# Optimization experiments

Hardware: AMD Instinct MI355X
Metric: run time of the kernel (lower is better)

The kernel has to match this reference:

```python
import jax, jax.numpy as jnp
import numpy as np

B, S, D, H = 4, 2048, 1024, 16
HD = D // H


def setup_inputs() -> dict:
    key = jax.random.key(0)
    ks = jax.random.split(key, 6)
    s = 1.0 / np.sqrt(D)
    return {
        "x": jax.random.normal(ks[0], (B, S, D), dtype=jnp.float32),
        "Wq": jax.random.normal(ks[1], (D, D), dtype=jnp.float32) * s,
        "Wk": jax.random.normal(ks[2], (D, D), dtype=jnp.float32) * s,
        "Wv": jax.random.normal(ks[3], (D, D), dtype=jnp.float32) * s,
        "Wo": jax.random.normal(ks[4], (D, D), dtype=jnp.float32) * s,
        "bo": jnp.zeros((D,), dtype=jnp.float32),
    }


def reference(x, Wq, Wk, Wv, Wo, bo):
    b, n, d = x.shape
    # QKV projections (torch Linear: x @ W.T, but weights here are stored as [d_in, d_out])
    q = (x @ Wq).reshape(b, n, H, HD).transpose(0, 2, 1, 3)  # [b,h,n,hd]
    k = (x @ Wk).reshape(b, n, H, HD).transpose(0, 2, 1, 3)
    v = (x @ Wv).reshape(b, n, H, HD).transpose(0, 2, 1, 3)
    scores = jnp.einsum("bhqd,bhkd->bhqk", q, k) / np.sqrt(HD)
    causal = jnp.tril(jnp.ones((n, n), dtype=bool))  # True = keep
    scores = jnp.where(causal, scores, -jnp.inf)
    attn = jax.nn.softmax(scores, axis=-1)
    ctx = jnp.einsum("bhqk,bhkd->bhqd", attn, v)
    ctx = ctx.transpose(0, 2, 1, 3).reshape(b, n, d)
    return ctx @ Wo + bo
```

## Files before the change

kernel.cpp:

```cpp
#include <hip/hip_runtime.h>
#include <hip/hip_bf16.h>

typedef __bf16 bf16;
typedef __bf16 bf16x4 __attribute__((ext_vector_type(4)));
typedef __bf16 bf16x8 __attribute__((ext_vector_type(8)));
typedef float f32x4 __attribute__((ext_vector_type(4)));

static constexpr int Bn = 4, Sn = 2048, Dn = 1024, Hn = 16, HDn = 64;
static constexpr int Mn = Bn * Sn;

__device__ __forceinline__ void gload_lds16(const void* g, void* l) {
  __builtin_amdgcn_global_load_lds(
      (const __attribute__((address_space(1))) unsigned int*)g,
      (__attribute__((address_space(3))) unsigned int*)l, 16, 0, 0);
}

__global__ void cvt_x_kernel(const float* __restrict__ x, bf16* __restrict__ xb, int n8) {
  int i = blockIdx.x * blockDim.x + threadIdx.x;
  if (i >= n8) return;
  const float4* p = reinterpret_cast<const float4*>(x) + (size_t)i * 2;
  float4 a = p[0], b = p[1];
  bf16x8 v;
  v[0] = (bf16)a.x; v[1] = (bf16)a.y; v[2] = (bf16)a.z; v[3] = (bf16)a.w;
  v[4] = (bf16)b.x; v[5] = (bf16)b.y; v[6] = (bf16)b.z; v[7] = (bf16)b.w;
  *(reinterpret_cast<bf16x8*>(xb) + i) = v;
}

struct alignas(8) B4 { bf16 e[4]; };

__global__ void transpose_w_kernel(const float* __restrict__ W0, const float* __restrict__ W1,
                                   const float* __restrict__ W2, const float* __restrict__ W3,
                                   bf16* __restrict__ WtQKV, bf16* __restrict__ Wot) {
  __shared__ bf16 tile[64][65];
  const int which = blockIdx.z;
  const float* W = (which == 0) ? W0 : (which == 1) ? W1 : (which == 2) ? W2 : W3;
  bf16* out = (which < 3) ? (WtQKV + (size_t)which * 1024 * 1024) : Wot;
  const int k0 = blockIdx.y * 64, n0 = blockIdx.x * 64;
  const int t = threadIdx.x;
  const int tr = t >> 4, tc = (t & 15) * 4;
#pragma unroll
  for (int rr = 0; rr < 4; ++rr) {
    const int row = rr * 16 + tr;
    float4 v = *reinterpret_cast<const float4*>(&W[(size_t)(k0 + row) * 1024 + n0 + tc]);
    tile[row][tc + 0] = (bf16)v.x; tile[row][tc + 1] = (bf16)v.y;
    tile[row][tc + 2] = (bf16)v.z; tile[row][tc + 3] = (bf16)v.w;
  }
  __syncthreads();
#pragma unroll
  for (int rr = 0; rr < 4; ++rr) {
    const int row = rr * 16 + tr;
    B4 o;
#pragma unroll
    for (int j = 0; j < 4; ++j) o.e[j] = tile[tc + j][row];
    *reinterpret_cast<B4*>(&out[(size_t)(n0 + row) * 1024 + k0 + tc]) = o;
  }
}

template <int MODE>
__global__ __launch_bounds__(256, 4)
void gemm_kernel(const bf16* __restrict__ A, const bf16* __restrict__ Bt,
                 float* __restrict__ Co, const float* __restrict__ bias,
                 bf16* __restrict__ Qo, bf16* __restrict__ Ko, bf16* __restrict__ Vto) {
  __shared__ bf16 Al[128 * 64];
  __shared__ bf16 Bl[128 * 64];
  const int tid = threadIdx.x;
  const int lane = tid & 63;
  const int wv = tid >> 6;
  const int wm = wv >> 1, wn = wv & 1;
  const int lr = lane & 15, lg = lane >> 4;
  const int m0 = blockIdx.y * 128, n0 = blockIdx.x * 128;

  int soff[4];
  const bf16* srcA[4];
  const bf16* srcB[4];
#pragma unroll
  for (int it = 0; it < 4; ++it) {
    const int elem = it * 2048 + tid * 8;
    const int row = elem >> 6;
    const int g = (elem >> 3) & 7;
    const int gs = g ^ (row & 7);
    soff[it] = elem;
    srcA[it] = A + (size_t)(m0 + row) * 1024 + gs * 8;
    srcB[it] = Bt + (size_t)(n0 + row) * 1024 + gs * 8;
  }

  f32x4 acc[4][4] = {};

  for (int ks = 0; ks < 16; ++ks) {
    const int kn = ks * 64;
#pragma unroll
    for (int it = 0; it < 4; ++it) {
      gload_lds16(srcA[it] + kn, (bf16*)&Al[0] + soff[it]);
      gload_lds16(srcB[it] + kn, (bf16*)&Bl[0] + soff[it]);
    }
    __syncthreads();
#pragma unroll
    for (int kk = 0; kk < 2; ++kk) {
      bf16x8 af[4], bfr[4];
#pragma unroll
      for (int i = 0; i < 4; ++i) {
        const int row = wm * 64 + i * 16 + lr;
        af[i] = *reinterpret_cast<const bf16x8*>(Al + row * 64 + (((kk * 4 + lg) ^ (row & 7)) << 3));
      }
#pragma unroll
      for (int i = 0; i < 4; ++i) {
        const int row = wn * 64 + i * 16 + lr;
        bfr[i] = *reinterpret_cast<const bf16x8*>(Bl + row * 64 + (((kk * 4 + lg) ^ (row & 7)) << 3));
      }
#pragma unroll
      for (int mi = 0; mi < 4; ++mi)
#pragma unroll
        for (int ni = 0; ni < 4; ++ni)
          acc[mi][ni] = __builtin_amdgcn_mfma_f32_16x16x32_bf16(af[mi], bfr[ni], acc[mi][ni], 0, 0, 0);
    }
    __syncthreads();
  }

  const int mrow = lg * 4;
  if (MODE == 0) {
    const int w = n0 >> 10;
    const int nl0 = n0 & 1023;
    if (w == 2) {
      const int b = m0 >> 11;
      const int sBase = (m0 & 2047) + wm * 64 + lg * 8;
#pragma unroll
      for (int ni = 0; ni < 4; ++ni) {
        const int nl = nl0 + wn * 64 + ni * 16 + lr;
        const int h = nl >> 6, hd = nl & 63;
        bf16* vbase = Vto + ((size_t)(b * 16 + h) * 64 + hd) * 2048;
#pragma unroll
        for (int mi = 0; mi < 4; ++mi) {
          B4 o;
#pragma unroll
          for (int i = 0; i < 4; ++i) o.e[i] = (bf16)acc[mi][ni][i];
          const int sNew = sBase + ((mi >> 1) << 5) + ((mi & 1) << 2);
          *reinterpret_cast<B4*>(&vbase[sNew]) = o;
        }
      }
    } else {
      const float fs = (w == 0) ? 0.18033688011112042f : 1.0f;
#pragma unroll
      for (int ni = 0; ni < 4; ++ni) {
        const int nl = nl0 + wn * 64 + ni * 16 + lr;
        const int h = nl >> 6, hd = nl & 63;
        bf16* dst = (w == 0) ? Qo : Ko;
#pragma unroll
        for (int mi = 0; mi < 4; ++mi) {
#pragma unroll
          for (int i = 0; i < 4; ++i) {
            const int m_g = m0 + wm * 64 + mi * 16 + mrow + i;
            const int b = m_g >> 11, s = m_g & 2047;
            dst[((size_t)(b * 16 + h) * 2048 + s) * 64 + hd] = (bf16)(acc[mi][ni][i] * fs);
          }
        }
      }
    }
  } else {
#pragma unroll
    for (int ni = 0; ni < 4; ++ni) {
      const int n_g = n0 + wn * 64 + ni * 16 + lr;
      const float bv = bias[n_g];
#pragma unroll
      for (int mi = 0; mi < 4; ++mi) {
#pragma unroll
        for (int i = 0; i < 4; ++i) {
          const int m_g = m0 + wm * 64 + mi * 16 + mrow + i;
          Co[(size_t)m_g * 1024 + n_g] = acc[mi][ni][i] + bv;
        }
      }
    }
  }
}

__device__ __forceinline__ unsigned int pack2(float lo, float hi) {
  union { bf16 bb[2]; unsigned int u; } c;
  c.bb[0] = (bf16)lo; c.bb[1] = (bf16)hi;
  return c.u;
}

__device__ __forceinline__ float smax_pack(const f32x4 (&sc)[4], unsigned int (&pk)[4][2],
                                           int kv0, int qrow, bool domask, int lg) {
  float p[4][4];
  float rs = 0.f;
#pragma unroll
  for (int ni = 0; ni < 4; ++ni)
#pragma unroll
    for (int r = 0; r < 4; ++r) {
      float pv = __builtin_amdgcn_exp2f(sc[ni][r]);
      if (domask && (kv0 + ni * 16 + lg * 4 + r > qrow)) pv = 0.f;
      p[ni][r] = pv;
      rs += pv;
    }
#pragma unroll
  for (int ni = 0; ni < 4; ++ni)
#pragma unroll
    for (int tt = 0; tt < 2; ++tt)
      pk[ni][tt] = pack2(p[ni][2 * tt], p[ni][2 * tt + 1]);
  return rs;
}

__global__ __launch_bounds__(256, 4)
void attn_kernel(const bf16* __restrict__ Q, const bf16* __restrict__ K,
                 const bf16* __restrict__ Vt, bf16* __restrict__ ctx) {
  __shared__ bf16 Kl[2][4096];
  __shared__ bf16 Vl[2][4096];
  const int tid = threadIdx.x, lane = tid & 63, wv = tid >> 6;
  const int lr = lane & 15, lg = lane >> 4, lk = lg * 8;
  const int bid = blockIdx.x;
  const int xcd = bid & 7, slot = bid >> 3;
  const int bh = xcd * 8 + (slot >> 4);
  const int pi = slot & 15;
  const bf16* Qh = Q + (size_t)bh * Sn * 64;
  const bf16* Kh = K + (size_t)bh * Sn * 64;
  const bf16* Vh = Vt + (size_t)bh * 64 * (size_t)Sn;
  const int b = bh >> 4, h = bh & 15;

  const int e0 = tid * 8, e1 = 2048 + tid * 8;
  const int r0 = e0 >> 6, r1 = e1 >> 6;
  const int gs0 = ((e0 >> 3) & 7) ^ (r0 & 7), gs1 = ((e1 >> 3) & 7) ^ (r1 & 7);
  const bf16* srcK0 = Kh + r0 * 64 + gs0 * 8;
  const bf16* srcK1 = Kh + r1 * 64 + gs1 * 8;
  const bf16* srcV0 = Vh + (size_t)r0 * Sn + gs0 * 8;
  const bf16* srcV1 = Vh + (size_t)r1 * Sn + gs1 * 8;

  for (int ph = 0; ph < 2; ++ph) {
    const int qtile = ph ? pi : 31 - pi;
    const int qw = qtile * 64 + wv * 16;
    const int qrow = qw + lr;
    bf16x8 aq[2];
#pragma unroll
    for (int kk = 0; kk < 2; ++kk)
      aq[kk] = *reinterpret_cast<const bf16x8*>(&Qh[(size_t)(qw + lr) * 64 + kk * 32 + lk]);

    f32x4 acc[4] = {};
    float lst = 0.f;
    const int nt = qtile + 1;

    gload_lds16(srcK0, &Kl[0][e0]);
    gload_lds16(srcK1, &Kl[0][e1]);
    gload_lds16(srcV0, &Vl[0][e0]);
    gload_lds16(srcV1, &Vl[0][e1]);
    __syncthreads();

    for (int t = 0; t < nt; ++t) {
      const int cur = t & 1;
      if (t + 1 < nt) {
        const int kvn = (t + 1) * 64;
        gload_lds16(srcK0 + kvn * 64, &Kl[cur ^ 1][e0]);
        gload_lds16(srcK1 + kvn * 64, &Kl[cur ^ 1][e1]);
        gload_lds16(srcV0 + kvn, &Vl[cur ^ 1][e0]);
        gload_lds16(srcV1 + kvn, &Vl[cur ^ 1][e1]);
      }
      const int kv0 = t * 64;
      const bf16* KlF = Kl[cur];
      const bf16* VlF = Vl[cur];

      f32x4 sc[4] = {};
#pragma unroll
      for (int kk = 0; kk < 2; ++kk) {
        bf16x8 ak[4];
#pragma unroll
        for (int ni = 0; ni < 4; ++ni) {
          const int row = ni * 16 + lr;
          ak[ni] = *reinterpret_cast<const bf16x8*>(KlF + row * 64 + (((kk * 4 + lg) ^ (row & 7)) << 3));
        }
        __builtin_amdgcn_s_setprio(1);
#pragma unroll
        for (int ni = 0; ni < 4; ++ni)
          sc[ni] = __builtin_amdgcn_mfma_f32_16x16x32_bf16(ak[ni], aq[kk], sc[ni], 0, 0, 0);
        __builtin_amdgcn_s_setprio(0);
      }
      unsigned int pk[4][2];
      {
        float rs = smax_pack(sc, pk, kv0, qrow, t == nt - 1, lg);
        rs += __shfl_xor(rs, 16);
        rs += __shfl_xor(rs, 32);
        lst += rs;
      }
#pragma unroll
      for (int kk = 0; kk < 2; ++kk) {
        union { unsigned int u[4]; bf16x8 v; } ap;
#pragma unroll
        for (int w = 0; w < 4; ++w) ap.u[w] = pk[2 * kk + (w >> 1)][w & 1];
        __builtin_amdgcn_s_setprio(1);
#pragma unroll
        for (int ni = 0; ni < 4; ++ni) {
          const int row = ni * 16 + lr;
          bf16x8 av = *reinterpret_cast<const bf16x8*>(VlF + row * 64 + (((kk * 4 + lg) ^ (row & 7)) << 3));
          acc[ni] = __builtin_amdgcn_mfma_f32_16x16x32_bf16(av, ap.v, acc[ni], 0, 0, 0);
        }
        __builtin_amdgcn_s_setprio(0);
      }
      __syncthreads();
    }

    const float inv = 1.f / lst;
    bf16* cbase = ctx + (((size_t)b * Sn + qw + lr) * 16 + h) * 64;
#pragma unroll
    for (int ni = 0; ni < 4; ++ni) {
      B4 o;
#pragma unroll
      for (int r = 0; r < 4; ++r) o.e[r] = (bf16)(acc[ni][r] * inv);
      *reinterpret_cast<B4*>(cbase + ni * 16 + lg * 4) = o;
    }
    __syncthreads();
  }
}

extern "C" void kernel_launch(void* const* d_in, const int* in_sizes, int n_in,
                              void* d_out, int out_size, void* d_ws, size_t ws_size,
                              hipStream_t stream) {
  const float* x = (const float*)d_in[0];
  const float* Wq = (const float*)d_in[1];
  const float* Wk = (const float*)d_in[2];
  const float* Wv = (const float*)d_in[3];
  const float* Wo = (const float*)d_in[4];
  const float* bo = (const float*)d_in[5];

  char* ws = (char*)d_ws;
  bf16* xb    = (bf16*)(ws);
  bf16* WtQKV = (bf16*)(ws + 0x1000000);
  bf16* Wot   = (bf16*)(ws + 0x1600000);
  bf16* Qb    = (bf16*)(ws + 0x1800000);
  bf16* Kb    = (bf16*)(ws + 0x2800000);
  bf16* Vtb   = (bf16*)(ws + 0x3800000);
  bf16* ctx   = xb;

  cvt_x_kernel<<<dim3(Mn * Dn / 8 / 256), dim3(256), 0, stream>>>(x, xb, Mn * Dn / 8);
  transpose_w_kernel<<<dim3(16, 16, 4), dim3(256), 0, stream>>>(Wq, Wk, Wv, Wo, WtQKV, Wot);
  gemm_kernel<0><<<dim3(24, 64), dim3(256), 0, stream>>>(xb, WtQKV, nullptr, nullptr, Qb, Kb, Vtb);
  attn_kernel<<<dim3(1024), dim3(256), 0, stream>>>(Qb, Kb, Vtb, ctx);
  gemm_kernel<1><<<dim3(8, 64), dim3(256), 0, stream>>>(ctx, Wot, (float*)d_out, bo,
                                                        nullptr, nullptr, nullptr);
}
```

Before: 160.4 us.

## Split KV tiles across waves with LDS reduction of partial attention outputs

Each of the four waves now handles all 64 query rows of the tile but only every fourth KV tile, instead of each wave owning 16 query rows and sweeping all KV tiles. Four KV tiles are staged into LDS per group, and at the end the partial accumulators and row sums are merged through a padded shared buffer. This lets each wave reuse its K/V fragments across four query sub-blocks and cuts the number of barriers per KV tile. In exchange it needs much more LDS (about 69KB) and more registers, so occupancy is lowered to 2 blocks per CU, there is no prefetch overlap between groups, and a reduction step is added. The softmax is unnormalized without a running max, so partial sums can be added directly.

```diff
diff --git a/kernel.cpp b/kernel.cpp
--- a/kernel.cpp
+++ b/kernel.cpp
@@ -199,11 +199,14 @@
   return rs;
 }
 
-__global__ __launch_bounds__(256, 4)
+__global__ __launch_bounds__(256, 2)
 void attn_kernel(const bf16* __restrict__ Q, const bf16* __restrict__ K,
                  const bf16* __restrict__ Vt, bf16* __restrict__ ctx) {
-  __shared__ bf16 Kl[2][4096];
-  __shared__ bf16 Vl[2][4096];
+  __shared__ char smem[70656];
+  bf16* stg = (bf16*)smem;
+  float* mrgF = (float*)smem;
+  float* lstb = (float*)(smem + 69632);
+
   const int tid = threadIdx.x, lane = tid & 63, wv = tid >> 6;
   const int lr = lane & 15, lg = lane >> 4, lk = lg * 8;
   const int bid = blockIdx.x;
@@ -225,83 +228,110 @@
 
   for (int ph = 0; ph < 2; ++ph) {
     const int qtile = ph ? pi : 31 - pi;
-    const int qw = qtile * 64 + wv * 16;
-    const int qrow = qw + lr;
-    bf16x8 aq[2];
-#pragma unroll
-    for (int kk = 0; kk < 2; ++kk)
-      aq[kk] = *reinterpret_cast<const bf16x8*>(&Qh[(size_t)(qw + lr) * 64 + kk * 32 + lk]);
-
-    f32x4 acc[4] = {};
-    float lst = 0.f;
+    const int q0 = qtile * 64;
+    bf16x8 aq[4][2];
+#pragma unroll
+    for (int qs = 0; qs < 4; ++qs)
+#pragma unroll
+      for (int kk = 0; kk < 2; ++kk)
+        aq[qs][kk] = *reinterpret_cast<const bf16x8*>(
+            &Qh[(size_t)(q0 + qs * 16 + lr) * 64 + kk * 32 + lk]);
+
+    f32x4 acc[4][4] = {};
+    float lst[4] = {0.f, 0.f, 0.f, 0.f};
     const int nt = qtile + 1;
-
-    gload_lds16(srcK0, &Kl[0][e0]);
-    gload_lds16(srcK1, &Kl[0][e1]);
-    gload_lds16(srcV0, &Vl[0][e0]);
-    gload_lds16(srcV1, &Vl[0][e1]);
+    const int ng = (nt + 3) >> 2;
+
+    for (int g = 0; g < ng; ++g) {
+#pragma unroll
+      for (int sl = 0; sl < 4; ++sl) {
+        int tw = 4 * g + sl;
+        tw = (tw < nt) ? tw : 0;
+        bf16* db = stg + sl * 8192;
+        gload_lds16(srcK0 + (size_t)tw * 4096, db + e0);
+        gload_lds16(srcK1 + (size_t)tw * 4096, db + e1);
+        gload_lds16(srcV0 + tw * 64, db + 4096 + e0);
+        gload_lds16(srcV1 + tw * 64, db + 4096 + e1);
+      }
+      __syncthreads();
+
+      const int t = 4 * g + wv;
+      if (t < nt) {
+        const bf16* KlF = stg + wv * 8192;
+        const bf16* VlF = KlF + 4096;
+        bf16x8 ak[2][4], av[2][4];
+#pragma unroll
+        for (int kk = 0; kk < 2; ++kk)
+#pragma unroll
+          for (int ni = 0; ni < 4; ++ni) {
+            const int row = ni * 16 + lr;
+            const int off = row * 64 + (((kk * 4 + lg) ^ (row & 7)) << 3);
+            ak[kk][ni] = *reinterpret_cast<const bf16x8*>(KlF + off);
+            av[kk][ni] = *reinterpret_cast<const bf16x8*>(VlF + off);
+          }
+        const int kv0 = t * 64;
+        const bool domask = (t == nt - 1);
+#pragma unroll
+        for (int qs = 0; qs < 4; ++qs) {
+          const int qrow = q0 + qs * 16 + lr;
+          f32x4 sc[4] = {};
+          __builtin_amdgcn_s_setprio(1);
+#pragma unroll
+          for (int kk = 0; kk < 2; ++kk)
+#pragma unroll
+            for (int ni = 0; ni < 4; ++ni)
+              sc[ni] = __builtin_amdgcn_mfma_f32_16x16x32_bf16(ak[kk][ni], aq[qs][kk], sc[ni], 0, 0, 0);
+          __builtin_amdgcn_s_setprio(0);
+          unsigned int pk[4][2];
+          float rs = smax_pack(sc, pk, kv0, qrow, domask, lg);
+          rs += __shfl_xor(rs, 16);
+          rs += __shfl_xor(rs, 32);
+          lst[qs] += rs;
+          __builtin_amdgcn_s_setprio(1);
+#pragma unroll
+          for (int kk = 0; kk < 2; ++kk) {
+            union { unsigned int u[4]; bf16x8 v; } ap;
+#pragma unroll
+            for (int w = 0; w < 4; ++w) ap.u[w] = pk[2 * kk + (w >> 1)][w & 1];
+#pragma unroll
+            for (int ni = 0; ni < 4; ++ni)
+              acc[qs][ni] = __builtin_amdgcn_mfma_f32_16x16x32_bf16(av[kk][ni], ap.v, acc[qs][ni], 0, 0, 0);
+          }
+          __builtin_amdgcn_s_setprio(0);
+        }
+      }
+      __syncthreads();
+    }
+
+#pragma unroll
+    for (int qs = 0; qs < 4; ++qs) {
+      float* rowp = mrgF + (size_t)(wv * 64 + qs * 16 + lr) * 68;
+#pragma unroll
+      for (int ni = 0; ni < 4; ++ni)
+        *reinterpret_cast<f32x4*>(rowp + ni * 16 + lg * 4) = acc[qs][ni];
+    }
+    if (lg == 0) {
+#pragma unroll
+      for (int qs = 0; qs < 4; ++qs) lstb[wv * 64 + qs * 16 + lr] = lst[qs];
+    }
     __syncthreads();
-
-    for (int t = 0; t < nt; ++t) {
-      const int cur = t & 1;
-      if (t + 1 < nt) {
-        const int kvn = (t + 1) * 64;
-        gload_lds16(srcK0 + kvn * 64, &Kl[cur ^ 1][e0]);
-        gload_lds16(srcK1 + kvn * 64, &Kl[cur ^ 1][e1]);
-        gload_lds16(srcV0 + kvn, &Vl[cur ^ 1][e0]);
-        gload_lds16(srcV1 + kvn, &Vl[cur ^ 1][e1]);
-      }
-      const int kv0 = t * 64;
-      const bf16* KlF = Kl[cur];
-      const bf16* VlF = Vl[cur];
-
-      f32x4 sc[4] = {};
-#pragma unroll
-      for (int kk = 0; kk < 2; ++kk) {
-        bf16x8 ak[4];
-#pragma unroll
-        for (int ni = 0; ni < 4; ++ni) {
-          const int row = ni * 16 + lr;
-          ak[ni] = *reinterpret_cast<const bf16x8*>(KlF + row * 64 + (((kk * 4 + lg) ^ (row & 7)) << 3));
-        }
-        __builtin_amdgcn_s_setprio(1);
-#pragma unroll
-        for (int ni = 0; ni < 4; ++ni)
-          sc[ni] = __builtin_amdgcn_mfma_f32_16x16x32_bf16(ak[ni], aq[kk], sc[ni], 0, 0, 0);
-        __builtin_amdgcn_s_setprio(0);
-      }
-      unsigned int pk[4][2];
-      {
-        float rs = smax_pack(sc, pk, kv0, qrow, t == nt - 1, lg);
-        rs += __shfl_xor(rs, 16);
-        rs += __shfl_xor(rs, 32);
-        lst += rs;
-      }
-#pragma unroll
-      for (int kk = 0; kk < 2; ++kk) {
-        union { unsigned int u[4]; bf16x8 v; } ap;
-#pragma unroll
-        for (int w = 0; w < 4; ++w) ap.u[w] = pk[2 * kk + (w >> 1)][w & 1];
-        __builtin_amdgcn_s_setprio(1);
-#pragma unroll
-        for (int ni = 0; ni < 4; ++ni) {
-          const int row = ni * 16 + lr;
-          bf16x8 av = *reinterpret_cast<const bf16x8*>(VlF + row * 64 + (((kk * 4 + lg) ^ (row & 7)) << 3));
-          acc[ni] = __builtin_amdgcn_mfma_f32_16x16x32_bf16(av, ap.v, acc[ni], 0, 0, 0);
-        }
-        __builtin_amdgcn_s_setprio(0);
-      }
-      __syncthreads();
-    }
-
-    const float inv = 1.f / lst;
-    bf16* cbase = ctx + (((size_t)b * Sn + qw + lr) * 16 + h) * 64;
-#pragma unroll
-    for (int ni = 0; ni < 4; ++ni) {
-      B4 o;
-#pragma unroll
-      for (int r = 0; r < 4; ++r) o.e[r] = (bf16)(acc[ni][r] * inv);
-      *reinterpret_cast<B4*>(cbase + ni * 16 + lg * 4) = o;
+    {
+      const int qloc = wv * 16 + lr;
+      const float lt = lstb[qloc] + lstb[64 + qloc] + lstb[128 + qloc] + lstb[192 + qloc];
+      const float inv = 1.f / lt;
+      bf16* cbase = ctx + (((size_t)b * Sn + q0 + qloc) * 16 + h) * 64;
+#pragma unroll
+      for (int ni = 0; ni < 4; ++ni) {
+        const int hoff = ni * 16 + lg * 4;
+        f32x4 s = *reinterpret_cast<const f32x4*>(mrgF + (size_t)qloc * 68 + hoff);
+#pragma unroll
+        for (int pw = 1; pw < 4; ++pw)
+          s += *reinterpret_cast<const f32x4*>(mrgF + (size_t)(pw * 64 + qloc) * 68 + hoff);
+        B4 o;
+#pragma unroll
+        for (int r = 0; r < 4; ++r) o.e[r] = (bf16)(s[r] * inv);
+        *reinterpret_cast<B4*>(cbase + hoff) = o;
+      }
     }
     __syncthreads();
   }
```

New measurement: 178.5 us. +11.3%, slower.

## Give each attention wave two query sub-tiles to reuse K/V fragments

Applied to the files above, without the earlier changes.

The attention kernel drops from four waves to two per block. Each wave now handles two 16-row query sub-tiles, so every K and V fragment read from LDS feeds two MFMAs. Each thread issues four async loads per buffer instead of two to fill the same K/V tile. This halves LDS read traffic per MFMA, at the cost of more registers per wave, fewer waves to hide latency, and a lower occupancy hint in launch_bounds.

```diff
diff --git a/kernel.cpp b/kernel.cpp
--- a/kernel.cpp
+++ b/kernel.cpp
@@ -199,7 +199,7 @@
   return rs;
 }
 
-__global__ __launch_bounds__(256, 4)
+__global__ __launch_bounds__(128, 2)
 void attn_kernel(const bf16* __restrict__ Q, const bf16* __restrict__ K,
                  const bf16* __restrict__ Vt, bf16* __restrict__ ctx) {
   __shared__ bf16 Kl[2][4096];
@@ -215,93 +215,120 @@
   const bf16* Vh = Vt + (size_t)bh * 64 * (size_t)Sn;
   const int b = bh >> 4, h = bh & 15;
 
-  const int e0 = tid * 8, e1 = 2048 + tid * 8;
-  const int r0 = e0 >> 6, r1 = e1 >> 6;
-  const int gs0 = ((e0 >> 3) & 7) ^ (r0 & 7), gs1 = ((e1 >> 3) & 7) ^ (r1 & 7);
-  const bf16* srcK0 = Kh + r0 * 64 + gs0 * 8;
-  const bf16* srcK1 = Kh + r1 * 64 + gs1 * 8;
-  const bf16* srcV0 = Vh + (size_t)r0 * Sn + gs0 * 8;
-  const bf16* srcV1 = Vh + (size_t)r1 * Sn + gs1 * 8;
+  int eo[4];
+  const bf16* sK[4];
+  const bf16* sV[4];
+#pragma unroll
+  for (int c = 0; c < 4; ++c) {
+    const int e = c * 1024 + tid * 8;
+    const int row = e >> 6;
+    const int gs = ((e >> 3) & 7) ^ (row & 7);
+    eo[c] = e;
+    sK[c] = Kh + row * 64 + gs * 8;
+    sV[c] = Vh + (size_t)row * Sn + gs * 8;
+  }
 
   for (int ph = 0; ph < 2; ++ph) {
     const int qtile = ph ? pi : 31 - pi;
-    const int qw = qtile * 64 + wv * 16;
-    const int qrow = qw + lr;
-    bf16x8 aq[2];
-#pragma unroll
-    for (int kk = 0; kk < 2; ++kk)
-      aq[kk] = *reinterpret_cast<const bf16x8*>(&Qh[(size_t)(qw + lr) * 64 + kk * 32 + lk]);
-
-    f32x4 acc[4] = {};
-    float lst = 0.f;
+    const int q0 = qtile * 64;
+    const int qw = q0 + wv * 16;
+    bf16x8 aq[2][2];
+#pragma unroll
+    for (int sub = 0; sub < 2; ++sub)
+#pragma unroll
+      for (int kk = 0; kk < 2; ++kk)
+        aq[sub][kk] = *reinterpret_cast<const bf16x8*>(
+            &Qh[(size_t)(qw + sub * 32 + lr) * 64 + kk * 32 + lk]);
+
+    f32x4 acc[2][4] = {};
+    float lst[2] = {0.f, 0.f};
     const int nt = qtile + 1;
 
-    gload_lds16(srcK0, &Kl[0][e0]);
-    gload_lds16(srcK1, &Kl[0][e1]);
-    gload_lds16(srcV0, &Vl[0][e0]);
-    gload_lds16(srcV1, &Vl[0][e1]);
+#pragma unroll
+    for (int c = 0; c < 4; ++c) {
+      gload_lds16(sK[c], &Kl[0][eo[c]]);
+      gload_lds16(sV[c], &Vl[0][eo[c]]);
+    }
     __syncthreads();
 
     for (int t = 0; t < nt; ++t) {
       const int cur = t & 1;
       if (t + 1 < nt) {
         const int kvn = (t + 1) * 64;
-        gload_lds16(srcK0 + kvn * 64, &Kl[cur ^ 1][e0]);
-        gload_lds16(srcK1 + kvn * 64, &Kl[cur ^ 1][e1]);
-        gload_lds16(srcV0 + kvn, &Vl[cur ^ 1][e0]);
-        gload_lds16(srcV1 + kvn, &Vl[cur ^ 1][e1]);
+#pragma unroll
+        for (int c = 0; c < 4; ++c) {
+          gload_lds16(sK[c] + (size_t)kvn * 64, &Kl[cur ^ 1][eo[c]]);
+          gload_lds16(sV[c] + kvn, &Vl[cur ^ 1][eo[c]]);
+        }
       }
       const int kv0 = t * 64;
       const bf16* KlF = Kl[cur];
       const bf16* VlF = Vl[cur];
-
-      f32x4 sc[4] = {};
-#pragma unroll
-      for (int kk = 0; kk < 2; ++kk) {
-        bf16x8 ak[4];
+      const bool domask = (t == nt - 1);
+
+      bf16x8 ak[2][4];
+#pragma unroll
+      for (int kk = 0; kk < 2; ++kk)
 #pragma unroll
         for (int ni = 0; ni < 4; ++ni) {
           const int row = ni * 16 + lr;
-          ak[ni] = *reinterpret_cast<const bf16x8*>(KlF + row * 64 + (((kk * 4 + lg) ^ (row & 7)) << 3));
-        }
-        __builtin_amdgcn_s_setprio(1);
-#pragma unroll
-        for (int ni = 0; ni < 4; ++ni)
-          sc[ni] = __builtin_amdgcn_mfma_f32_16x16x32_bf16(ak[ni], aq[kk], sc[ni], 0, 0, 0);
-        __builtin_amdgcn_s_setprio(0);
-      }
-      unsigned int pk[4][2];
+          ak[kk][ni] = *reinterpret_cast<const bf16x8*>(KlF + row * 64 + (((kk * 4 + lg) ^ (row & 7)) << 3));
+        }
+      f32x4 sc0[4] = {}, sc1[4] = {};
+      __builtin_amdgcn_s_setprio(1);
+#pragma unroll
+      for (int kk = 0; kk < 2; ++kk)
+#pragma unroll
+        for (int ni = 0; ni < 4; ++ni) {
+          sc0[ni] = __builtin_amdgcn_mfma_f32_16x16x32_bf16(ak[kk][ni], aq[0][kk], sc0[ni], 0, 0, 0);
+          sc1[ni] = __builtin_amdgcn_mfma_f32_16x16x32_bf16(ak[kk][ni], aq[1][kk], sc1[ni], 0, 0, 0);
+        }
+      __builtin_amdgcn_s_setprio(0);
+      unsigned int pk0[4][2], pk1[4][2];
       {
-        float rs = smax_pack(sc, pk, kv0, qrow, t == nt - 1, lg);
+        float rs = smax_pack(sc0, pk0, kv0, qw + lr, domask, lg);
         rs += __shfl_xor(rs, 16);
         rs += __shfl_xor(rs, 32);
-        lst += rs;
-      }
+        lst[0] += rs;
+      }
+      {
+        float rs = smax_pack(sc1, pk1, kv0, qw + 32 + lr, domask, lg);
+        rs += __shfl_xor(rs, 16);
+        rs += __shfl_xor(rs, 32);
+        lst[1] += rs;
+      }
+      __builtin_amdgcn_s_setprio(1);
 #pragma unroll
       for (int kk = 0; kk < 2; ++kk) {
-        union { unsigned int u[4]; bf16x8 v; } ap;
-#pragma unroll
-        for (int w = 0; w < 4; ++w) ap.u[w] = pk[2 * kk + (w >> 1)][w & 1];
-        __builtin_amdgcn_s_setprio(1);
+        union { unsigned int u[4]; bf16x8 v; } ap0, ap1;
+#pragma unroll
+        for (int w = 0; w < 4; ++w) {
+          ap0.u[w] = pk0[2 * kk + (w >> 1)][w & 1];
+          ap1.u[w] = pk1[2 * kk + (w >> 1)][w & 1];
+        }
 #pragma unroll
         for (int ni = 0; ni < 4; ++ni) {
           const int row = ni * 16 + lr;
           bf16x8 av = *reinterpret_cast<const bf16x8*>(VlF + row * 64 + (((kk * 4 + lg) ^ (row & 7)) << 3));
-          acc[ni] = __builtin_amdgcn_mfma_f32_16x16x32_bf16(av, ap.v, acc[ni], 0, 0, 0);
-        }
-        __builtin_amdgcn_s_setprio(0);
-      }
+          acc[0][ni] = __builtin_amdgcn_mfma_f32_16x16x32_bf16(av, ap0.v, acc[0][ni], 0, 0, 0);
+          acc[1][ni] = __builtin_amdgcn_mfma_f32_16x16x32_bf16(av, ap1.v, acc[1][ni], 0, 0, 0);
+        }
+      }
+      __builtin_amdgcn_s_setprio(0);
       __syncthreads();
     }
 
-    const float inv = 1.f / lst;
-    bf16* cbase = ctx + (((size_t)b * Sn + qw + lr) * 16 + h) * 64;
-#pragma unroll
-    for (int ni = 0; ni < 4; ++ni) {
-      B4 o;
-#pragma unroll
-      for (int r = 0; r < 4; ++r) o.e[r] = (bf16)(acc[ni][r] * inv);
-      *reinterpret_cast<B4*>(cbase + ni * 16 + lg * 4) = o;
+#pragma unroll
+    for (int sub = 0; sub < 2; ++sub) {
+      const float inv = 1.f / lst[sub];
+      bf16* cbase = ctx + (((size_t)b * Sn + qw + sub * 32 + lr) * 16 + h) * 64;
+#pragma unroll
+      for (int ni = 0; ni < 4; ++ni) {
+        B4 o;
+#pragma unroll
+        for (int r = 0; r < 4; ++r) o.e[r] = (bf16)(acc[sub][ni][r] * inv);
+        *reinterpret_cast<B4*>(cbase + ni * 16 + lg * 4) = o;
+      }
     }
     __syncthreads();
   }
@@ -329,7 +356,7 @@
   cvt_x_kernel<<<dim3(Mn * Dn / 8 / 256), dim3(256), 0, stream>>>(x, xb, Mn * Dn / 8);
   transpose_w_kernel<<<dim3(16, 16, 4), dim3(256), 0, stream>>>(Wq, Wk, Wv, Wo, WtQKV, Wot);
   gemm_kernel<0><<<dim3(24, 64), dim3(256), 0, stream>>>(xb, WtQKV, nullptr, nullptr, Qb, Kb, Vtb);
-  attn_kernel<<<dim3(1024), dim3(256), 0, stream>>>(Qb, Kb, Vtb, ctx);
+  attn_kernel<<<dim3(1024), dim3(128), 0, stream>>>(Qb, Kb, Vtb, ctx);
   gemm_kernel<1><<<dim3(8, 64), dim3(256), 0, stream>>>(ctx, Wot, (float*)d_out, bo,
                                                         nullptr, nullptr, nullptr);
 }
```

Result: no change. 163.1 us (+1.7%).
